# Performance work log

Hardware: AMD Instinct MI355X
Metric: run time of the kernel (lower is better)

## Reference

```python
import math
import jax, jax.numpy as jnp
import numpy as np

MODEL_DIM = 256
NUM_HEADS = 8
HEAD_DIM = MODEL_DIM // NUM_HEADS
B, S = 4, 2048


def setup_inputs() -> dict:
    key = jax.random.key(0)
    ks = jax.random.split(key, 9)
    d = MODEL_DIM
    lim = 1.0 / math.sqrt(d)  # torch nn.Linear init range
    def lin(k):
        k1, k2 = jax.random.split(k)
        W = jax.random.uniform(k1, (d, d), jnp.float32, -lim, lim)
        b = jax.random.uniform(k2, (d,), jnp.float32, -lim, lim)
        return W, b
    Wq, bq = lin(ks[0])
    Wk, bk = lin(ks[1])
    Wv, bv = lin(ks[2])
    Wo, bo = lin(ks[3])
    q = jax.random.normal(ks[4], (B, S, d), jnp.float32)
    q_mask = jnp.ones((B, S), dtype=bool)
    return {"q": q, "q_mask": q_mask, "Wq": Wq, "bq": bq, "Wk": Wk, "bk": bk,
            "Wv": Wv, "bv": bv, "Wo": Wo, "bo": bo}


def reference(q, q_mask, Wq, bq, Wk, bk, Wv, bv, Wo, bo):
    b, s, d = q.shape
    h, hd = NUM_HEADS, HEAD_DIM
    # merge_masks: kv_mask defaults to q_mask (self-attention), pad_mask -> float bias
    pad = q_mask[:, :, None] & q_mask[:, None, :]            # [b, s, s] recv x send
    bias = jnp.where(pad, 0.0, -jnp.inf).astype(q.dtype)      # additive attn bias
    # projections, split heads: [b, s, d] -> [b, h, s, hd]
    def proj(x, W, bb):
        return (x @ W.T + bb).reshape(b, s, h, hd).transpose(0, 2, 1, 3)
    qh = proj(q, Wq, bq)
    kh = proj(q, Wk, bk)
    vh = proj(q, Wv, bv)
    # NOTE: original scales by sqrt(model_dim), not sqrt(head_dim)
    qh = qh / math.sqrt(d)
    scores = jnp.einsum('bhqe,bhke->bhqk', qh, kh) + bias[:, None, :, :]
    attn = jax.nn.softmax(scores, axis=-1)
    out = jnp.einsum('bhqk,bhke->bhqe', attn, vh)             # [b, h, s, hd]
    out = out.transpose(0, 2, 1, 3).reshape(b, s, d)
    out = out @ Wo.T + bo
    return jnp.nan_to_num(out)
```

## Files before the change

kernel.cpp:

```cpp
#include <hip/hip_runtime.h>
#include <hip/hip_bf16.h>

typedef __attribute__((ext_vector_type(8))) short bf16x8;
typedef __attribute__((ext_vector_type(4))) short bf16x4;
typedef __attribute__((ext_vector_type(4))) float f32x4;
typedef unsigned short ushort_t;
typedef unsigned int uint_t;

__device__ __forceinline__ ushort_t f2bf(float f) {
  unsigned int u = __builtin_bit_cast(unsigned int, f);
  u += 0x7fffu + ((u >> 16) & 1u);
  return (ushort_t)(u >> 16);
}

__device__ __forceinline__ bf16x8 cvt8(f32x4 a, f32x4 b) {
  bf16x8 r;
  r[0] = (short)f2bf(a[0]); r[1] = (short)f2bf(a[1]);
  r[2] = (short)f2bf(a[2]); r[3] = (short)f2bf(a[3]);
  r[4] = (short)f2bf(b[0]); r[5] = (short)f2bf(b[1]);
  r[6] = (short)f2bf(b[2]); r[7] = (short)f2bf(b[3]);
  return r;
}

#if __has_builtin(__builtin_amdgcn_exp2f)
#define EXP2(x) __builtin_amdgcn_exp2f(x)
#else
#define EXP2(x) __expf(0.69314718056f * (x))
#endif

__device__ __forceinline__ f32x4 mfma16(bf16x4 a, bf16x4 b, f32x4 c) {
#if __has_builtin(__builtin_amdgcn_mfma_f32_16x16x16bf16_1k)
  return __builtin_amdgcn_mfma_f32_16x16x16bf16_1k(a, b, c, 0, 0, 0);
#else
  f32x4 d;
  asm volatile(
      "v_mfma_f32_16x16x16_bf16 %0, %1, %2, %3\n\ts_nop 7\n\ts_nop 7"
      : "=&v"(d)
      : "v"(a), "v"(b), "v"(c));
  return d;
#endif
}

__device__ __forceinline__ void gld_lds16(const void* g, void* l) {
  __builtin_amdgcn_global_load_lds(
      (const __attribute__((address_space(1))) unsigned int*)g,
      (__attribute__((address_space(3))) unsigned int*)l, 16, 0, 0);
}

__global__ __launch_bounds__(256) void prep2_kernel(
    const float* __restrict__ x, const float* __restrict__ Wq,
    const float* __restrict__ Wk, const float* __restrict__ Wv,
    const float* __restrict__ Wo, ushort_t* __restrict__ xb,
    ushort_t* __restrict__ Wb, ushort_t* __restrict__ Wob) {
  const int blk = blockIdx.x;
  const float* src;
  ushort_t* dst;
  int base;
  if (blk < 1024)      { src = x;  dst = xb;          base = blk * 2048; }
  else if (blk < 1056) { src = Wq; dst = Wb;          base = (blk - 1024) * 2048; }
  else if (blk < 1088) { src = Wk; dst = Wb + 65536;  base = (blk - 1056) * 2048; }
  else if (blk < 1120) { src = Wv; dst = Wb + 131072; base = (blk - 1088) * 2048; }
  else                 { src = Wo; dst = Wob;         base = (blk - 1120) * 2048; }
  const int i = base + threadIdx.x * 8;
  const f32x4 a = *(const f32x4*)(src + i);
  const f32x4 b = *(const f32x4*)(src + i + 4);
  *(bf16x8*)(dst + i) = cvt8(a, b);
}

__global__ __launch_bounds__(256) void qkv2_kernel(
    const ushort_t* __restrict__ xb, const ushort_t* __restrict__ Wb,
    const float* __restrict__ bq, const float* __restrict__ bk,
    const float* __restrict__ bv, ushort_t* __restrict__ qh,
    ushort_t* __restrict__ kh, ushort_t* __restrict__ vT) {
  __shared__ ushort_t Xs[2][2][2048], Ws[2][2][2048];
  const int tid = threadIdx.x;
  const int wid = tid >> 6, lane = tid & 63;
  const int l15 = lane & 15, lg = lane >> 4;
  const int row0 = blockIdx.x * 64;
  const int col0 = blockIdx.y * 64;
  const bool isV = (blockIdx.y >= 8);
  const char* XpB = (const char*)(xb + (size_t)row0 * 256);
  const char* WpB = (const char*)(Wb + (size_t)col0 * 256);
  const uint_t gsrc =
      (uint_t)((tid >> 2) * 512 + (((tid & 3) ^ ((tid >> 3) & 3)) << 4));
  const int kswz = (lg ^ ((l15 >> 1) & 3)) << 4;
  const int mrow = (wid >> 1) * 32, ncol = (wid & 1) * 32;
  f32x4 acc[2][2] = {};

#define STG(buf, t)                                                   \
  {                                                                   \
    gld_lds16(XpB + (t) * 64 + gsrc, (char*)Xs[buf][0] + wid * 1024); \
    gld_lds16(XpB + ((t) + 1) * 64 + gsrc,                            \
              (char*)Xs[buf][1] + wid * 1024);                        \
    gld_lds16(WpB + (t) * 64 + gsrc, (char*)Ws[buf][0] + wid * 1024); \
    gld_lds16(WpB + ((t) + 1) * 64 + gsrc,                            \
              (char*)Ws[buf][1] + wid * 1024);                        \
  }

#define CMP(XS, WS)                                                          \
  {                                                                          \
    const char* xs = (const char*)XS;                                        \
    const char* ws = (const char*)WS;                                        \
    bf16x8 af[2], bfr[2];                                                    \
    _Pragma("unroll") for (int m = 0; m < 2; ++m) af[m] =                    \
        *(const bf16x8*)(xs + (mrow + m * 16 + l15) * 64 + kswz);            \
    _Pragma("unroll") for (int n = 0; n < 2; ++n) bfr[n] =                   \
        *(const bf16x8*)(ws + (ncol + n * 16 + l15) * 64 + kswz);            \
    if (isV) {                                                               \
      _Pragma("unroll") for (int m = 0; m < 2; ++m) _Pragma("unroll")        \
          for (int n = 0; n < 2; ++n) acc[m][n] =                            \
              __builtin_amdgcn_mfma_f32_16x16x32_bf16(bfr[n], af[m],         \
                                                      acc[m][n], 0, 0, 0);   \
    } else {                                                                 \
      _Pragma("unroll") for (int m = 0; m < 2; ++m) _Pragma("unroll")        \
          for (int n = 0; n < 2; ++n) acc[m][n] =                            \
              __builtin_amdgcn_mfma_f32_16x16x32_bf16(af[m], bfr[n],         \
                                                      acc[m][n], 0, 0, 0);   \
    }                                                                        \
  }

  STG(0, 0)
  __syncthreads();
  for (int t = 0; t < 8; t += 4) {
    if (t + 2 < 8) STG(1, t + 2)
    CMP(Xs[0][0], Ws[0][0])
    CMP(Xs[0][1], Ws[0][1])
    __syncthreads();
    if (t + 4 < 8) STG(0, t + 4)
    CMP(Xs[1][0], Ws[1][0])
    CMP(Xs[1][1], Ws[1][1])
    __syncthreads();
  }
#undef STG
#undef CMP

  if (!isV) {
#pragma unroll
    for (int n = 0; n < 2; ++n) {
      const int gcol = col0 + ncol + n * 16 + l15;
      const bool isQ = (gcol < 256);
      const int c = gcol & 255;
      const float bias = (isQ ? bq : bk)[c];
      ushort_t* dst = isQ ? qh : kh;
      const float scale = isQ ? 0.0901684400f : 1.0f;
      const int h = c >> 5, e = c & 31;
#pragma unroll
      for (int m = 0; m < 2; ++m)
#pragma unroll
        for (int j = 0; j < 4; ++j) {
          const int grow = row0 + mrow + m * 16 + lg * 4 + j;
          const int b_ = grow >> 11, s_ = grow & 2047;
          dst[(size_t)((b_ * 8 + h) * 2048 + s_) * 32 + e] =
              f2bf((acc[m][n][j] + bias) * scale);
        }
    }
  } else {
#pragma unroll
    for (int n = 0; n < 2; ++n)
#pragma unroll
      for (int j = 0; j < 4; ++j) {
        const int c = col0 + ncol - 512 + n * 16 + lg * 4 + j;
        const float bias = bv[c];
        const int h = c >> 5, e = c & 31;
#pragma unroll
        for (int m = 0; m < 2; ++m) {
          const int grow = row0 + mrow + m * 16 + l15;
          const int b_ = grow >> 11, s_ = grow & 2047;
          vT[((size_t)(b_ * 8 + h) * 32 + e) * 2048 + s_] =
              f2bf(acc[m][n][j] + bias);
        }
      }
  }
}

__global__ __launch_bounds__(256) void oproj2_kernel(
    const ushort_t* __restrict__ a, const ushort_t* __restrict__ Wob,
    const float* __restrict__ bo, float* __restrict__ out) {
  __shared__ ushort_t Xs[2][2][2048], Ws[2][2][2048];
  const int tid = threadIdx.x;
  const int wid = tid >> 6, lane = tid & 63;
  const int l15 = lane & 15, lg = lane >> 4;
  const int row0 = blockIdx.x * 64;
  const int col0 = blockIdx.y * 64;
  const char* XpB = (const char*)(a + (size_t)row0 * 256);
  const char* WpB = (const char*)(Wob + (size_t)col0 * 256);
  const uint_t gsrc =
      (uint_t)((tid >> 2) * 512 + (((tid & 3) ^ ((tid >> 3) & 3)) << 4));
  const int kswz = (lg ^ ((l15 >> 1) & 3)) << 4;
  const int mrow = (wid >> 1) * 32, ncol = (wid & 1) * 32;
  f32x4 acc[2][2] = {};

#define STG(buf, t)                                                   \
  {                                                                   \
    gld_lds16(XpB + (t) * 64 + gsrc, (char*)Xs[buf][0] + wid * 1024); \
    gld_lds16(XpB + ((t) + 1) * 64 + gsrc,                            \
              (char*)Xs[buf][1] + wid * 1024);                        \
    gld_lds16(WpB + (t) * 64 + gsrc, (char*)Ws[buf][0] + wid * 1024); \
    gld_lds16(WpB + ((t) + 1) * 64 + gsrc,                            \
              (char*)Ws[buf][1] + wid * 1024);                        \
  }

#define CMP(XS, WS)                                                          \
  {                                                                          \
    const char* xs = (const char*)XS;                                        \
    const char* ws = (const char*)WS;                                        \
    bf16x8 af[2], bfr[2];                                                    \
    _Pragma("unroll") for (int m = 0; m < 2; ++m) af[m] =                    \
        *(const bf16x8*)(xs + (mrow + m * 16 + l15) * 64 + kswz);            \
    _Pragma("unroll") for (int n = 0; n < 2; ++n) bfr[n] =                   \
        *(const bf16x8*)(ws + (ncol + n * 16 + l15) * 64 + kswz);            \
    _Pragma("unroll") for (int m = 0; m < 2; ++m) _Pragma("unroll")          \
        for (int n = 0; n < 2; ++n) acc[m][n] =                              \
            __builtin_amdgcn_mfma_f32_16x16x32_bf16(af[m], bfr[n],           \
                                                    acc[m][n], 0, 0, 0);     \
  }

  STG(0, 0)
  __syncthreads();
  for (int t = 0; t < 8; t += 4) {
    if (t + 2 < 8) STG(1, t + 2)
    CMP(Xs[0][0], Ws[0][0])
    CMP(Xs[0][1], Ws[0][1])
    __syncthreads();
    if (t + 4 < 8) STG(0, t + 4)
    CMP(Xs[1][0], Ws[1][0])
    CMP(Xs[1][1], Ws[1][1])
    __syncthreads();
  }
#undef STG
#undef CMP

#pragma unroll
  for (int n = 0; n < 2; ++n) {
    const int gcol = col0 + ncol + n * 16 + l15;
    const float bias = bo[gcol];
#pragma unroll
    for (int m = 0; m < 2; ++m)
#pragma unroll
      for (int j = 0; j < 4; ++j) {
        const int grow = row0 + mrow + m * 16 + lg * 4 + j;
        out[(size_t)grow * 256 + gcol] = acc[m][n][j] + bias;
      }
  }
}

__global__ __launch_bounds__(256) void attn_kernel(
    const ushort_t* __restrict__ qh, const ushort_t* __restrict__ kh,
    const ushort_t* __restrict__ vT, ushort_t* __restrict__ ao) {
  __shared__ ushort_t Ksh[2][2][2048];
  __shared__ ushort_t Vsh[2][2][2048];
  const int tid = threadIdx.x;
  const int wid = tid >> 6, lane = tid & 63;
  const int l15 = lane & 15, lg = lane >> 4;
  const int bh = blockIdx.x & 31;
  const int qg = blockIdx.x >> 5;
  const int q0 = qg * 64 + wid * 16;
  const ushort_t* Qp = qh + ((size_t)bh * 2048 + q0) * 32;
  const char* KpB = (const char*)(kh + (size_t)bh * 2048 * 32);
  const char* VpB = (const char*)(vT + (size_t)bh * 32 * 2048);
  const bf16x8 qf = *(const bf16x8*)(Qp + l15 * 32 + lg * 8);
  const bf16x4 ones = {(short)0x3F80, (short)0x3F80, (short)0x3F80,
                       (short)0x3F80};
  f32x4 oacc[2] = {};
  f32x4 dacc = {0.f, 0.f, 0.f, 0.f};

  const uint_t ksrc =
      (uint_t)((tid >> 2) * 64 + (((tid & 3) ^ ((tid >> 3) & 3)) << 4));
  const uint_t vsrc = (uint_t)((tid >> 3) * 4096 +
                               (((tid & 7) ^ ((tid >> 3) & 7)) << 4));
  const int kswz = (lg ^ ((l15 >> 1) & 3)) << 4;
  const int vlo = (lg & 1) << 3;
  const int e7 = l15 & 7;

#define STAGE(buf, half, tile)                                            \
  {                                                                       \
    gld_lds16(KpB + (tile) * 4096 + ksrc,                                 \
              (char*)Ksh[buf][half] + wid * 1024);                        \
    gld_lds16(VpB + (tile) * 128 + vsrc,                                  \
              (char*)Vsh[buf][half] + wid * 1024);                        \
  }

#define COMPUTE(K, V)                                                          \
  {                                                                            \
    const char* kb = (const char*)K;                                           \
    const char* vb = (const char*)V;                                           \
    _Pragma("unroll") for (int t4 = 0; t4 < 4; ++t4) {                         \
      const bf16x8 kf = *(const bf16x8*)(kb + (t4 * 16 + l15) * 64 + kswz);    \
      const f32x4 sf = __builtin_amdgcn_mfma_f32_16x16x32_bf16(                \
          kf, qf, (f32x4){0, 0, 0, 0}, 0, 0, 0);                               \
      bf16x4 pa;                                                               \
      {                                                                        \
        union { bf16x4 v4; __hip_bfloat162 h2[2]; } u;                         \
        u.h2[0] = __float22bfloat162_rn(make_float2(EXP2(sf[0]), EXP2(sf[1])));\
        u.h2[1] = __float22bfloat162_rn(make_float2(EXP2(sf[2]), EXP2(sf[3])));\
        pa = u.v4;                                                             \
      }                                                                        \
      dacc = mfma16(pa, ones, dacc);                                           \
      const int vchunk = (((t4 * 2 + (lg >> 1)) ^ e7) << 4) + vlo;             \
      const bf16x4 v0 = *(const bf16x4*)(vb + l15 * 128 + vchunk);             \
      const bf16x4 v1 = *(const bf16x4*)(vb + (16 + l15) * 128 + vchunk);      \
      oacc[0] = mfma16(pa, v0, oacc[0]);                                       \
      oacc[1] = mfma16(pa, v1, oacc[1]);                                       \
    }                                                                          \
  }

  STAGE(0, 0, 0)
  STAGE(0, 1, 1)
  __syncthreads();
  for (int t = 0; t < 32; t += 4) {
    if (t + 2 < 32) {
      STAGE(1, 0, t + 2)
      STAGE(1, 1, t + 3)
    }
    __builtin_amdgcn_s_setprio(1);
    COMPUTE(Ksh[0][0], Vsh[0][0])
    COMPUTE(Ksh[0][1], Vsh[0][1])
    __builtin_amdgcn_s_setprio(0);
    __syncthreads();
    if (t + 4 < 32) {
      STAGE(0, 0, t + 4)
      STAGE(0, 1, t + 5)
    }
    __builtin_amdgcn_s_setprio(1);
    COMPUTE(Ksh[1][0], Vsh[1][0])
    COMPUTE(Ksh[1][1], Vsh[1][1])
    __builtin_amdgcn_s_setprio(0);
    __syncthreads();
  }
#undef STAGE
#undef COMPUTE

  const int b_ = bh >> 3, h = bh & 7;
#pragma unroll
  for (int j = 0; j < 4; ++j) {
    const float rd = 1.0f / dacc[j];
    const int s_ = q0 + 4 * lg + j;
#pragma unroll
    for (int et = 0; et < 2; ++et) {
      const int col = h * 32 + et * 16 + l15;
      ao[((size_t)(b_ * 2048) + s_) * 256 + col] = f2bf(oacc[et][j] * rd);
    }
  }
}

extern "C" void kernel_launch(void* const* d_in, const int* in_sizes, int n_in,
                              void* d_out, int out_size, void* d_ws,
                              size_t ws_size, hipStream_t stream) {
  const float* q = (const float*)d_in[0];
  const float* Wq = (const float*)d_in[2];
  const float* bq = (const float*)d_in[3];
  const float* Wk = (const float*)d_in[4];
  const float* bk = (const float*)d_in[5];
  const float* Wv = (const float*)d_in[6];
  const float* bv = (const float*)d_in[7];
  const float* Wo = (const float*)d_in[8];
  const float* bo = (const float*)d_in[9];

  ushort_t* qh = (ushort_t*)d_ws;
  ushort_t* kh = qh + (size_t)2097152;
  ushort_t* vT = kh + (size_t)2097152;
  ushort_t* xb_ao = vT + (size_t)2097152;
  ushort_t* Wb = xb_ao + (size_t)2097152;
  ushort_t* Wob = Wb + (size_t)196608;
  float* out = (float*)d_out;

  prep2_kernel<<<dim3(1152), 256, 0, stream>>>(q, Wq, Wk, Wv, Wo, xb_ao, Wb,
                                               Wob);
  qkv2_kernel<<<dim3(128, 12), 256, 0, stream>>>(xb_ao, Wb, bq, bk, bv, qh,
                                                 kh, vT);
  attn_kernel<<<dim3(1024), 256, 0, stream>>>(qh, kh, vT, xb_ao);
  oproj2_kernel<<<dim3(128, 4), 256, 0, stream>>>(xb_ao, Wob, bo, out);
}
```

Baseline: 59.16 us.

## Switch attention to 32x32x16 MFMA with 32-query warp tiles

Attention now has each wave handle 32 queries instead of 16 and uses 32x32x16 bf16 MFMAs for QK^T, PV and the row-sum accumulation. P fragments are rearranged in registers with v_permlane32_swap instead of going through LDS, and the grid is halved to 512 blocks. This doubles K/V reuse per LDS load and cuts the MFMA instruction count, at the cost of more accumulator registers (f32x16) and fewer blocks to spread across the CUs.

Measured after the change: 60.36 us. 1.02x slower.

```diff
diff --git a/kernel.cpp b/kernel.cpp
--- a/kernel.cpp
+++ b/kernel.cpp
@@ -4,6 +4,7 @@
 typedef __attribute__((ext_vector_type(8))) short bf16x8;
 typedef __attribute__((ext_vector_type(4))) short bf16x4;
 typedef __attribute__((ext_vector_type(4))) float f32x4;
+typedef __attribute__((ext_vector_type(16))) float f32x16;
 typedef unsigned short ushort_t;
 typedef unsigned int uint_t;
 
@@ -28,17 +29,10 @@
 #define EXP2(x) __expf(0.69314718056f * (x))
 #endif
 
-__device__ __forceinline__ f32x4 mfma16(bf16x4 a, bf16x4 b, f32x4 c) {
-#if __has_builtin(__builtin_amdgcn_mfma_f32_16x16x16bf16_1k)
-  return __builtin_amdgcn_mfma_f32_16x16x16bf16_1k(a, b, c, 0, 0, 0);
-#else
-  f32x4 d;
-  asm volatile(
-      "v_mfma_f32_16x16x16_bf16 %0, %1, %2, %3\n\ts_nop 7\n\ts_nop 7"
-      : "=&v"(d)
-      : "v"(a), "v"(b), "v"(c));
-  return d;
-#endif
+__device__ __forceinline__ uint_t pkexp(float a, float b) {
+  union { __hip_bfloat162 h2; uint_t u; } cv;
+  cv.h2 = __float22bfloat162_rn(make_float2(EXP2(a), EXP2(b)));
+  return cv.u;
 }
 
 __device__ __forceinline__ void gld_lds16(const void* g, void* l) {
@@ -244,33 +238,34 @@
   }
 }
 
-__global__ __launch_bounds__(256) void attn_kernel(
+__global__ __launch_bounds__(256, 2) void attn_kernel(
     const ushort_t* __restrict__ qh, const ushort_t* __restrict__ kh,
     const ushort_t* __restrict__ vT, ushort_t* __restrict__ ao) {
   __shared__ ushort_t Ksh[2][2][2048];
   __shared__ ushort_t Vsh[2][2][2048];
   const int tid = threadIdx.x;
   const int wid = tid >> 6, lane = tid & 63;
-  const int l15 = lane & 15, lg = lane >> 4;
+  const int l31 = lane & 31, hi = lane >> 5;
+  const int e7_ = l31 & 7;
   const int bh = blockIdx.x & 31;
   const int qg = blockIdx.x >> 5;
-  const int q0 = qg * 64 + wid * 16;
-  const ushort_t* Qp = qh + ((size_t)bh * 2048 + q0) * 32;
+  const int q0w = qg * 128 + wid * 32;
+  const ushort_t* Qp = qh + ((size_t)bh * 2048 + q0w) * 32;
   const char* KpB = (const char*)(kh + (size_t)bh * 2048 * 32);
   const char* VpB = (const char*)(vT + (size_t)bh * 32 * 2048);
-  const bf16x8 qf = *(const bf16x8*)(Qp + l15 * 32 + lg * 8);
-  const bf16x4 ones = {(short)0x3F80, (short)0x3F80, (short)0x3F80,
-                       (short)0x3F80};
-  f32x4 oacc[2] = {};
-  f32x4 dacc = {0.f, 0.f, 0.f, 0.f};
+  const bf16x8 qf0 = *(const bf16x8*)(Qp + l31 * 32 + 8 * hi);
+  const bf16x8 qf1 = *(const bf16x8*)(Qp + l31 * 32 + 16 + 8 * hi);
+  const bf16x8 ones8 = {(short)0x3F80, (short)0x3F80, (short)0x3F80,
+                        (short)0x3F80, (short)0x3F80, (short)0x3F80,
+                        (short)0x3F80, (short)0x3F80};
+  const f32x16 z16 = {};
+  f32x16 oacc = {};
+  f32x16 dacc = {};
 
   const uint_t ksrc =
       (uint_t)((tid >> 2) * 64 + (((tid & 3) ^ ((tid >> 3) & 3)) << 4));
   const uint_t vsrc = (uint_t)((tid >> 3) * 4096 +
                                (((tid & 7) ^ ((tid >> 3) & 7)) << 4));
-  const int kswz = (lg ^ ((l15 >> 1) & 3)) << 4;
-  const int vlo = (lg & 1) << 3;
-  const int e7 = l15 & 7;
 
 #define STAGE(buf, half, tile)                                            \
   {                                                                       \
@@ -284,23 +279,32 @@
   {                                                                            \
     const char* kb = (const char*)K;                                           \
     const char* vb = (const char*)V;                                           \
-    _Pragma("unroll") for (int t4 = 0; t4 < 4; ++t4) {                         \
-      const bf16x8 kf = *(const bf16x8*)(kb + (t4 * 16 + l15) * 64 + kswz);    \
-      const f32x4 sf = __builtin_amdgcn_mfma_f32_16x16x32_bf16(                \
-          kf, qf, (f32x4){0, 0, 0, 0}, 0, 0, 0);                               \
-      bf16x4 pa;                                                               \
-      {                                                                        \
-        union { bf16x4 v4; __hip_bfloat162 h2[2]; } u;                         \
-        u.h2[0] = __float22bfloat162_rn(make_float2(EXP2(sf[0]), EXP2(sf[1])));\
-        u.h2[1] = __float22bfloat162_rn(make_float2(EXP2(sf[2]), EXP2(sf[3])));\
-        pa = u.v4;                                                             \
+    _Pragma("unroll") for (int b32 = 0; b32 < 2; ++b32) {                      \
+      const int krow = b32 * 32 + l31;                                         \
+      const int ks2 = (krow >> 1) & 3;                                         \
+      const bf16x8 kf0 =                                                       \
+          *(const bf16x8*)(kb + krow * 64 + ((hi ^ ks2) << 4));                \
+      const bf16x8 kf1 =                                                       \
+          *(const bf16x8*)(kb + krow * 64 + (((2 + hi) ^ ks2) << 4));          \
+      f32x16 sf =                                                              \
+          __builtin_amdgcn_mfma_f32_32x32x16_bf16(kf0, qf0, z16, 0, 0, 0);     \
+      sf = __builtin_amdgcn_mfma_f32_32x32x16_bf16(kf1, qf1, sf, 0, 0, 0);     \
+      _Pragma("unroll") for (int w = 0; w < 2; ++w) {                          \
+        uint_t A0 = pkexp(sf[8 * w + 0], sf[8 * w + 1]);                       \
+        uint_t A1 = pkexp(sf[8 * w + 2], sf[8 * w + 3]);                       \
+        uint_t B0 = pkexp(sf[8 * w + 4], sf[8 * w + 5]);                       \
+        uint_t B1 = pkexp(sf[8 * w + 6], sf[8 * w + 7]);                       \
+        asm volatile("v_permlane32_swap_b32 %0, %1" : "+v"(A0), "+v"(B0));     \
+        asm volatile("v_permlane32_swap_b32 %0, %1" : "+v"(A1), "+v"(B1));     \
+        union { uint_t u[4]; bf16x8 v8; } pu;                                  \
+        pu.u[0] = A0; pu.u[1] = A1; pu.u[2] = B0; pu.u[3] = B1;                \
+        const int vchunk = (4 * b32 + 2 * w + hi) ^ e7_;                       \
+        const bf16x8 vf = *(const bf16x8*)(vb + l31 * 128 + (vchunk << 4));    \
+        oacc = __builtin_amdgcn_mfma_f32_32x32x16_bf16(pu.v8, vf, oacc,        \
+                                                       0, 0, 0);               \
+        dacc = __builtin_amdgcn_mfma_f32_32x32x16_bf16(pu.v8, ones8, dacc,     \
+                                                       0, 0, 0);               \
       }                                                                        \
-      dacc = mfma16(pa, ones, dacc);                                           \
-      const int vchunk = (((t4 * 2 + (lg >> 1)) ^ e7) << 4) + vlo;             \
-      const bf16x4 v0 = *(const bf16x4*)(vb + l15 * 128 + vchunk);             \
-      const bf16x4 v1 = *(const bf16x4*)(vb + (16 + l15) * 128 + vchunk);      \
-      oacc[0] = mfma16(pa, v0, oacc[0]);                                       \
-      oacc[1] = mfma16(pa, v1, oacc[1]);                                       \
     }                                                                          \
   }
 
@@ -332,14 +336,10 @@
 
   const int b_ = bh >> 3, h = bh & 7;
 #pragma unroll
-  for (int j = 0; j < 4; ++j) {
-    const float rd = 1.0f / dacc[j];
-    const int s_ = q0 + 4 * lg + j;
-#pragma unroll
-    for (int et = 0; et < 2; ++et) {
-      const int col = h * 32 + et * 16 + l15;
-      ao[((size_t)(b_ * 2048) + s_) * 256 + col] = f2bf(oacc[et][j] * rd);
-    }
+  for (int r = 0; r < 16; ++r) {
+    const float rd = 1.0f / dacc[r];
+    const int s_ = q0w + (r & 3) + 8 * (r >> 2) + 4 * hi;
+    ao[((size_t)(b_ * 2048) + s_) * 256 + h * 32 + l31] = f2bf(oacc[r] * rd);
   }
 }
 
@@ -368,6 +368,6 @@
                                                Wob);
   qkv2_kernel<<<dim3(128, 12), 256, 0, stream>>>(xb_ao, Wb, bq, bk, bv, qh,
                                                  kh, vT);
-  attn_kernel<<<dim3(1024), 256, 0, stream>>>(qh, kh, vT, xb_ao);
+  attn_kernel<<<dim3(512), 256, 0, stream>>>(qh, kh, vT, xb_ao);
   oproj2_kernel<<<dim3(128, 4), 256, 0, stream>>>(xb_ao, Wob, bo, out);
 }
```

## Replace double-buffered K/V staging with four-slot ring and vmcnt-based waits

Applied to the files above, without the earlier changes.

Restructures the attention kernel's K/V shared-memory pipeline from two double-buffered half-pairs into a four-slot ring buffer, staging one tile two iterations ahead. Instead of full __syncthreads, it waits on a partial vmcnt count plus a raw barrier, so later loads remain in flight during compute. This aims to overlap global-to-LDS transfers with MFMA work more continuously, at the cost of one barrier per tile instead of one per two tiles.

Result: slower. 62.17 us (+5.1%).

```diff
diff --git a/kernel.cpp b/kernel.cpp
--- a/kernel.cpp
+++ b/kernel.cpp
@@ -247,8 +247,8 @@
 __global__ __launch_bounds__(256) void attn_kernel(
     const ushort_t* __restrict__ qh, const ushort_t* __restrict__ kh,
     const ushort_t* __restrict__ vT, ushort_t* __restrict__ ao) {
-  __shared__ ushort_t Ksh[2][2][2048];
-  __shared__ ushort_t Vsh[2][2][2048];
+  __shared__ ushort_t Ksh[4][2048];
+  __shared__ ushort_t Vsh[4][2048];
   const int tid = threadIdx.x;
   const int wid = tid >> 6, lane = tid & 63;
   const int l15 = lane & 15, lg = lane >> 4;
@@ -272,12 +272,10 @@
   const int vlo = (lg & 1) << 3;
   const int e7 = l15 & 7;
 
-#define STAGE(buf, half, tile)                                            \
-  {                                                                       \
-    gld_lds16(KpB + (tile) * 4096 + ksrc,                                 \
-              (char*)Ksh[buf][half] + wid * 1024);                        \
-    gld_lds16(VpB + (tile) * 128 + vsrc,                                  \
-              (char*)Vsh[buf][half] + wid * 1024);                        \
+#define STAGE(slot, tile)                                              \
+  {                                                                    \
+    gld_lds16(KpB + (tile) * 4096 + ksrc, (char*)Ksh[slot] + wid * 1024); \
+    gld_lds16(VpB + (tile) * 128 + vsrc, (char*)Vsh[slot] + wid * 1024);  \
   }
 
 #define COMPUTE(K, V)                                                          \
@@ -304,31 +302,33 @@
     }                                                                          \
   }
 
-  STAGE(0, 0, 0)
-  STAGE(0, 1, 1)
-  __syncthreads();
-  for (int t = 0; t < 32; t += 4) {
-    if (t + 2 < 32) {
-      STAGE(1, 0, t + 2)
-      STAGE(1, 1, t + 3)
-    }
+#define WAITB(lit)                                          \
+  {                                                         \
+    asm volatile("s_waitcnt vmcnt(" lit ")" ::: "memory");  \
+    __builtin_amdgcn_s_barrier();                           \
+    __builtin_amdgcn_sched_barrier(0);                      \
+  }
+
+  STAGE(0, 0)
+  STAGE(1, 1)
+  for (int t = 0; t < 30; ++t) {
+    STAGE((t + 2) & 3, t + 2)
+    WAITB("4")
     __builtin_amdgcn_s_setprio(1);
-    COMPUTE(Ksh[0][0], Vsh[0][0])
-    COMPUTE(Ksh[0][1], Vsh[0][1])
+    COMPUTE(Ksh[t & 3], Vsh[t & 3])
     __builtin_amdgcn_s_setprio(0);
-    __syncthreads();
-    if (t + 4 < 32) {
-      STAGE(0, 0, t + 4)
-      STAGE(0, 1, t + 5)
-    }
-    __builtin_amdgcn_s_setprio(1);
-    COMPUTE(Ksh[1][0], Vsh[1][0])
-    COMPUTE(Ksh[1][1], Vsh[1][1])
-    __builtin_amdgcn_s_setprio(0);
-    __syncthreads();
-  }
+  }
+  WAITB("2")
+  __builtin_amdgcn_s_setprio(1);
+  COMPUTE(Ksh[2], Vsh[2])
+  __builtin_amdgcn_s_setprio(0);
+  WAITB("0")
+  __builtin_amdgcn_s_setprio(1);
+  COMPUTE(Ksh[3], Vsh[3])
+  __builtin_amdgcn_s_setprio(0);
 #undef STAGE
 #undef COMPUTE
+#undef WAITB
 
   const int b_ = bh >> 3, h = bh & 7;
 #pragma unroll
```
